# Optimization experiments

Measured on AMD Instinct MI355X. Metric: run time of the kernel, lower is better.

Reference implementation:

```python
import jax, jax.numpy as jnp
import numpy as np

TWO_THIRDS = 2.0 / 3.0
SEVENTEEN_SIXTHS = 17.0 / 6.0


def _grid():
    # torch: cat(-flip(logspace(-2,2,100)**2), [0], logspace(-2,2,100)**2) -> 201 points
    gp = jnp.logspace(-2.0, 2.0, 100, dtype=jnp.float32) ** 2
    return jnp.concatenate([-gp[::-1], jnp.zeros((1,), jnp.float32), gp])


def _trapz_w(x):
    # trapezoidal quadrature weights so that trapz(f, x) == sum(f * w)
    dx = jnp.diff(x)
    w = jnp.zeros_like(x)
    return w.at[:-1].add(0.5 * dx).at[1:].add(0.5 * dx)


def setup_inputs() -> dict:
    key = jax.random.key(0)
    k1k, kyk, kzk = jax.random.split(key, 3)
    k1 = jnp.sort(jax.random.uniform(k1k, (512,), jnp.float32, 0.01, 1.0))  # positive wavenumbers
    dy = jax.random.uniform(kyk, (64,), jnp.float32, 0.0, 50.0)  # spanwise separations [m]
    dz = jax.random.uniform(kzk, (64,), jnp.float32, 0.0, 50.0)  # vertical separations [m]
    return {
        "k1_input": k1,
        "Delta_y": dy,
        "Delta_z": dz,
        "logLengthScale": jnp.float32(np.log(0.7 * 42.0)),
        "logTimeScale": jnp.float32(np.log(3.9)),
        "logMagnitude": jnp.float32(0.0),
    }


def reference(k1_input, Delta_y, Delta_z, logLengthScale, logTimeScale, logMagnitude):
    L = jnp.exp(logLengthScale)
    T = jnpp = jnp.exp(logTimeScale)
    M = jnp.exp(logMagnitude)
    k2g = _grid()  # [201]
    k3g = _grid()  # [201]
    # broadcasted meshgrid (never materialize a 4D stacked k tensor)
    k1 = k1_input[:, None, None]   # [Nk1,1,1]
    k2 = k2g[None, :, None]        # [1,201,1]
    k3 = k3g[None, None, :]        # [1,1,201]
    kk = k1 * k1 + k2 * k2 + k3 * k3
    # EddyLifetime 'TwoThird': beta = T * (L*|k|)^{-2/3}
    beta = T * (L * jnp.sqrt(kk)) ** (-TWO_THIRDS)
    k30 = k3 + beta * k1
    kk0 = k1 * k1 + k2 * k2 + k30 * k30
    k0L = L * jnp.sqrt(kk0)
    # von Karman energy spectrum at distorted wavevector
    E0 = M * k0L ** 4 / (1.0 + k0L * k0L) ** SEVENTEEN_SIXTHS
    # RDT spectral tensor, 11-component (module uses Phi[0] for Phi11, Phi33 and Phi13)
    s = k1 * k1 + k2 * k2
    C1 = beta * k1 * k1 * (kk0 - 2.0 * k30 * k30 + beta * k1 * k30) / (kk * s)
    C2 = k2 * kk0 / s ** 1.5 * jnp.arctan2(beta * k1 * jnp.sqrt(s), kk0 - k30 * k1 * beta)
    zeta1 = C1 - (k2 / k1) * C2
    Phi11 = E0 / (4.0 * jnp.pi * kk0 * kk0) * (
        kk0 - k1 * k1 - 2.0 * k1 * k30 * zeta1 + s * zeta1 * zeta1
    )  # [Nk1,201,201]
    # double trapezoid over (k2,k3) as weighted sums
    w2 = _trapz_w(k2g)
    w3 = _trapz_w(k3g)
    F1 = jnp.einsum('aij,i,j->a', Phi11, w2, w3)  # = F3
    den = jnp.sqrt(F1 * F1)
    # exp(i(k2*dy + k3*dz)) is separable -> factor the nested loop into two einsums
    Pw = (Phi11 * w2[None, :, None] * w3[None, None, :]).astype(jnp.complex64)
    E3 = jnp.exp(1j * k3g[:, None] * Delta_z[None, :])  # [201,Nz]
    E2 = jnp.exp(1j * k2g[:, None] * Delta_y[None, :])  # [201,Ny]
    A = jnp.einsum('aij,jz->aiz', Pw, E3)   # [Nk1,201,Nz]
    I = jnp.einsum('aiz,iy->ayz', A, E2)    # [Nk1,Ny,Nz]
    return jnp.real(I) / den[:, None, None]
```

## Files before the change

kernel.cpp:

```cpp
#include <hip/hip_runtime.h>
#include <math.h>

#define BLOCK 256
#define LOG2_10 3.3219280948873623f
#define PI_F 3.14159265358979f
#define INV2PI 0.15915494309189535f
#define PW_SCALE 256.0f

#define SP 128
#define SA 128
#define FT 56

typedef _Float16 half8 __attribute__((ext_vector_type(8)));
typedef _Float16 half2v __attribute__((ext_vector_type(2)));
typedef float f32x4 __attribute__((ext_vector_type(4)));
typedef float v2f  __attribute__((ext_vector_type(2)));
typedef int   i32x4 __attribute__((ext_vector_type(4)));

__device__ __forceinline__ v2f v2(float a, float b) { v2f r; r.x = a; r.y = b; return r; }

__device__ __forceinline__ float fast_cos(float x_rev) {
    return __builtin_amdgcn_cosf(__builtin_amdgcn_fractf(x_rev));
}

__device__ __forceinline__ v2f atan2_pos_pk(float yv, v2f x) {
    float ax0 = __builtin_fabsf(x.x), ax1 = __builtin_fabsf(x.y);
    float mn0 = fminf(ax0, yv), mx0 = fmaxf(ax0, yv);
    float mn1 = fminf(ax1, yv), mx1 = fmaxf(ax1, yv);
    v2f a = v2(mn0 * __builtin_amdgcn_rcpf(mx0), mn1 * __builtin_amdgcn_rcpf(mx1));
    v2f t = a * a;
    v2f p = ((((( -0.0117212f * t + 0.05265332f) * t - 0.11643287f) * t
              + 0.19354346f) * t - 0.33262347f) * t + 0.99997726f) * a;
    float p0 = (yv > ax0) ? (1.57079632679f - p.x) : p.x;
    float p1 = (yv > ax1) ? (1.57079632679f - p.y) : p.y;
    p0 = (x.x < 0.0f) ? (3.14159265359f - p0) : p0;
    p1 = (x.y < 0.0f) ? (3.14159265359f - p1) : p1;
    return v2(p0, p1);
}

__device__ __forceinline__ float phi_pair_pk(float k1, float k1sq, float n2k1, float Ttk1,
                                             float L2, float s, float sqs, float k2sc, float g) {
    const float kk  = g * g + s;
    const float bk1 = Ttk1 * __builtin_amdgcn_exp2f((-1.0f/3.0f) * __builtin_amdgcn_logf(L2 * kk));
    const float Qh  = bk1 * g;
    const float sg  = 2.0f * s - kk;
    const float cc  = (bk1 * k1) * __builtin_amdgcn_rcpf(kk * s);
    const float yv  = bk1 * sqs;
    const float R   = bk1 * bk1 + kk;
    const v2f x   = v2(kk - Qh, kk + Qh);
    const v2f C1  = cc * v2(sg + Qh, sg - Qh);
    const v2f kk0 = v2(R - 2.0f * Qh, R + 2.0f * Qh);
    const v2f th  = atan2_pos_pk(yv, x);
    const v2f vv  = L2 * kk0 + 1.0f;
    const v2f p   = v2(__builtin_amdgcn_exp2f((-17.0f/6.0f) * __builtin_amdgcn_logf(vv.x)),
                       __builtin_amdgcn_exp2f((-17.0f/6.0f) * __builtin_amdgcn_logf(vv.y)));
    const v2f z   = C1 - k2sc * (kk0 * th);
    const v2f k30 = v2(bk1 - g, bk1 + g);
    const v2f qq  = (s * z + n2k1 * k30) * z + (kk0 - k1sq);
    const v2f r   = p * qq;
    return r.x + r.y;
}

__device__ __forceinline__ float phi_pair_cheap(float k1sq, float L2, float s, float g) {
    const float kk = g * g + s;
    const float p  = __builtin_amdgcn_exp2f((-17.0f/6.0f) *
                     __builtin_amdgcn_logf(fmaf(L2, kk, 1.0f)));
    return 2.0f * p * (kk - k1sq);
}

__global__ __launch_bounds__(BLOCK, 2)
void spectral_kernel(const float* __restrict__ k1_in,
                     const float* __restrict__ dy_in,
                     const float* __restrict__ dz_in,
                     const float* __restrict__ plogL,
                     const float* __restrict__ plogT,
                     const float* __restrict__ plogM,
                     float* __restrict__ out)
{
    __shared__ __attribute__((aligned(16))) _Float16 s_phiT[2 * 32 * SP];
    __shared__ __attribute__((aligned(16))) _Float16 s_B3T[64 * SP];
    __shared__ __attribute__((aligned(16))) _Float16 s_A2[64 * SA];
    __shared__ float  s_grid[204];
    __shared__ float2 s_gw[204];
    __shared__ float  s_dy[64], s_dz[64];
    __shared__ float  s_red[8];

    const int t    = threadIdx.x;
    const int a    = blockIdx.x;
    const int lane = t & 63;
    const int w    = t >> 6;
    const int n16  = lane & 15;
    const int quad = lane >> 4;

    const float L  = expf(plogL[0]);
    const float Tt = expf(plogT[0]);
    const float M  = expf(plogM[0]);
    const float L2 = L * L;
    const float L4 = L2 * L2;
    const float k1   = k1_in[a];
    const float k1sq = k1 * k1;
    const float n2k1 = -2.0f * k1;
    const float Ttk1 = Tt * k1;
    const float rk1  = __builtin_amdgcn_rcpf(k1);
    const float cM0  = (M * 0.25f / PI_F) * PW_SCALE * L4;

    if (t < 204) {
        int tt = min(t, 200);
        float v;
        if (tt < 100)       v = -exp2f(LOG2_10 * (-4.0f + 8.0f * (float)(99 - tt) * (1.0f/99.0f)));
        else if (tt == 100) v = 0.0f;
        else                v =  exp2f(LOG2_10 * (-4.0f + 8.0f * (float)(tt - 101) * (1.0f/99.0f)));
        s_grid[t] = v;
    }
    if (t < 64) { s_dy[t] = dy_in[t]; s_dz[t] = dz_in[t]; }
    __syncthreads();

    if (t < 204) {
        float wv = 0.0f;
        if (t == 0)          wv = 0.5f * (s_grid[1] - s_grid[0]);
        else if (t < 200)    wv = 0.5f * (s_grid[t+1] - s_grid[t-1]);
        else if (t == 200)   wv = 0.5f * (s_grid[200] - s_grid[199]);
        s_gw[t] = make_float2(s_grid[t], wv);
    }
    {
        const int jjp = lane;
        const int jj0 = 2 * jjp, jj1 = jj0 + 1;
        if (jj0 < 96) {
            const float g0 = s_grid[100 + jj0];
            const float g1 = s_grid[100 + jj1];
            const int jjg  = jjp >> 2;
            for (int m = 0; m < 16; ++m) {
                int z = w + 4 * m;
                float dzr = s_dz[z] * INV2PI;
                float c0 = (jj0 < 88) ? fast_cos(g0 * dzr) : 0.0f;
                float c1 = (jj1 < 88) ? fast_cos(g1 * dzr) : 0.0f;
                half2v pr; pr.x = (_Float16)c0; pr.y = (_Float16)c1;
                *(half2v*)&s_B3T[z * SP + ((jjg ^ (z & 7)) << 3) + (jj0 & 7)] = pr;
            }
        }
    }
    {
        float dyr = s_dy[lane] * INV2PI;
        for (int k = 0; k < 12; ++k) {
            int iip = w + 4 * k;
            int i0 = 2 * iip, i1 = i0 + 1;
            float c0 = (i0 < 88) ? fast_cos(s_grid[100 + i0] * dyr) : 0.0f;
            float c1 = (i1 < 88) ? fast_cos(s_grid[100 + i1] * dyr) : 0.0f;
            half2v pr; pr.x = (_Float16)c0; pr.y = (_Float16)c1;
            int off = lane * SA + (((iip >> 2) ^ (lane & 7)) << 3) + ((iip & 3) << 1);
            *(half2v*)&s_A2[off] = pr;
        }
    }
    __syncthreads();

    float f1 = 0.0f;
    f32x4 acc2[4];
    #pragma unroll
    for (int i = 0; i < 4; ++i) acc2[i] = (f32x4){0.f, 0.f, 0.f, 0.f};

    auto do_full = [&](int ii, int jj, int row, _Float16* bp) {
        float k2  = s_gw[100 + ii].x;
        float cM  = cM0 * (s_gw[100 + ii].y * ((ii == 0) ? 1.0f : 2.0f));
        float s   = k1sq + k2 * k2;
        float rs  = __builtin_amdgcn_rsqf(s);
        float sqs = s * rs;
        float k2sc = (k2 * rk1) * k2 * (rs * rs * rs);
        float2 gwv = s_gw[100 + jj];
        float w3s = (jj == 0) ? 0.5f * gwv.y : gwv.y;
        float val = phi_pair_pk(k1, k1sq, n2k1, Ttk1, L2, s, sqs, k2sc, gwv.x) * cM * w3s;
        f1 += val;
        bp[row * SP + (((jj >> 3) ^ (row & 7)) << 3) + (jj & 7)] = (_Float16)val;
    };
    auto do_cheap = [&](int ii, int jj, int row, _Float16* bp) {
        float k2 = s_gw[100 + ii].x;
        float cM = cM0 * (s_gw[100 + ii].y * ((ii == 0) ? 1.0f : 2.0f));
        float s  = k1sq + k2 * k2;
        float2 gwv = s_gw[100 + jj];
        float w3s = (jj == 0) ? 0.5f * gwv.y : gwv.y;
        float val = phi_pair_cheap(k1sq, L2, s, gwv.x) * cM * w3s;
        f1 += val;
        bp[row * SP + (((jj >> 3) ^ (row & 7)) << 3) + (jj & 7)] = (_Float16)val;
    };

    {
        _Float16* bp = s_phiT;
        if (t < 32) {
            half8 zz = {};
            *(half8*)&bp[t * SP + ((11 ^ (t & 7)) << 3)] = zz;
        }
        #pragma unroll 2
        for (int m = 0; m < 7; ++m) {
            int e = t + 256 * m;
            int row = e / FT, jj = e - row * FT;
            do_full(row, jj, row, bp);
        }
        #pragma unroll
        for (int m = 0; m < 4; ++m) {
            int e = t + 256 * m;
            int row = e >> 5, jj = FT + (e & 31);
            do_cheap(row, jj, row, bp);
        }
    }
    __syncthreads();

    for (int c = 0; c < 3; ++c) {
        const _Float16* rp = s_phiT + (c & 1) * (32 * SP);

        f32x4 acc1[2];
        acc1[0] = (f32x4){0.f,0.f,0.f,0.f};
        acc1[1] = (f32x4){0.f,0.f,0.f,0.f};
        {
            const int arow0 = n16;
            const int arow1 = 16 + n16;
            const int brow  = w * 16 + n16;
            #pragma unroll
            for (int ks = 0; ks < 3; ++ks) {
                int kg = ks * 4 + quad;
                half8 af0 = *(const half8*)&rp[arow0 * SP + ((kg ^ (arow0 & 7)) << 3)];
                half8 af1 = *(const half8*)&rp[arow1 * SP + ((kg ^ (arow1 & 7)) << 3)];
                half8 bf  = *(const half8*)&s_B3T[brow * SP + ((kg ^ (brow & 7)) << 3)];
                acc1[0] = __builtin_amdgcn_mfma_f32_16x16x32_f16(af0, bf, acc1[0], 0, 0, 0);
                acc1[1] = __builtin_amdgcn_mfma_f32_16x16x32_f16(af1, bf, acc1[1], 0, 0, 0);
            }
        }

        half8 bf2;
        {
            half2v hA0; hA0.x = (_Float16)acc1[0].x; hA0.y = (_Float16)acc1[0].y;
            half2v hA1; hA1.x = (_Float16)acc1[0].z; hA1.y = (_Float16)acc1[0].w;
            half2v hB0; hB0.x = (_Float16)acc1[1].x; hB0.y = (_Float16)acc1[1].y;
            half2v hB1; hB1.x = (_Float16)acc1[1].z; hB1.y = (_Float16)acc1[1].w;
            int pkA0 = __builtin_bit_cast(int, hA0);
            int pkA1 = __builtin_bit_cast(int, hA1);
            int pkB0 = __builtin_bit_cast(int, hB0);
            int pkB1 = __builtin_bit_cast(int, hB1);
            const int addr_a = (((quad & 1) << 5) + n16) << 2;
            const int addr_b = addr_a + 64;
            int a0 = __builtin_amdgcn_ds_bpermute(addr_a, pkA0);
            int b0 = __builtin_amdgcn_ds_bpermute(addr_a, pkB0);
            int a1 = __builtin_amdgcn_ds_bpermute(addr_a, pkA1);
            int b1 = __builtin_amdgcn_ds_bpermute(addr_a, pkB1);
            int a2 = __builtin_amdgcn_ds_bpermute(addr_b, pkA0);
            int b2 = __builtin_amdgcn_ds_bpermute(addr_b, pkB0);
            int a3 = __builtin_amdgcn_ds_bpermute(addr_b, pkA1);
            int b3 = __builtin_amdgcn_ds_bpermute(addr_b, pkB1);
            const bool lo = (quad < 2);
            i32x4 wv;
            wv.x = lo ? a0 : b0;
            wv.y = lo ? a1 : b1;
            wv.z = lo ? a2 : b2;
            wv.w = lo ? a3 : b3;
            bf2 = __builtin_bit_cast(half8, wv);
        }

        {
            const int G = c * 4 + quad;
            #pragma unroll
            for (int yb = 0; yb < 4; ++yb) {
                int yrow = yb * 16 + n16;
                half8 a2f = *(const half8*)&s_A2[yrow * SA + ((G ^ (yrow & 7)) << 3)];
                acc2[yb] = __builtin_amdgcn_mfma_f32_16x16x32_f16(a2f, bf2, acc2[yb], 0, 0, 0);
            }
        }

        if (c == 0) {
            _Float16* bp = s_phiT + 32 * SP;
            if (t < 32) {
                half8 zz = {};
                *(half8*)&bp[t * SP + ((11 ^ (t & 7)) << 3)] = zz;
            }
            #pragma unroll 2
            for (int m = 0; m < 6; ++m) {
                int e = t + 256 * m;
                if (e < 1344) {
                    int row = e / FT, jj = e - row * FT;
                    do_full(32 + row, jj, row, bp);
                }
            }
            #pragma unroll
            for (int m = 0; m < 6; ++m) {
                int e = t + 256 * m;
                if (e < 1472) {
                    int row, jj;
                    if (e < 768) { row = e >> 5; jj = FT + (e & 31); }
                    else { int e2 = e - 768; row = 24 + e2 / 88; jj = e2 - (row - 24) * 88; }
                    do_cheap(32 + row, jj, row, bp);
                }
            }
        } else if (c == 1) {
            _Float16* bp = s_phiT;
            if (t < 120) {
                int row, slot;
                if (t < 96) { row = 24 + t / 12; int g = t - (row - 24) * 12; slot = g ^ (row & 7); }
                else        { row = t - 96;      slot = 11 ^ (row & 7); }
                half8 zz = {};
                *(half8*)&bp[row * SP + (slot << 3)] = zz;
            }
            #pragma unroll
            for (int m = 0; m < 9; ++m) {
                int e = t + 256 * m;
                if (e < 2112) {
                    int row = e / 88, jj = e - row * 88;
                    do_cheap(64 + row, jj, row, bp);
                }
            }
        }
        __syncthreads();
    }

    float v = f1;
    #pragma unroll
    for (int off = 32; off > 0; off >>= 1) v += __shfl_down(v, off, 64);
    if (lane == 0) s_red[w] = v;
    __syncthreads();
    if (t == 0) s_red[4] = 1.0f / fabsf(s_red[0] + s_red[1] + s_red[2] + s_red[3]);
    __syncthreads();
    const float rden = s_red[4];

    float* op = out + ((size_t)a << 12) + (w * 16 + n16);
    #pragma unroll
    for (int yb = 0; yb < 4; ++yb) {
        #pragma unroll
        for (int r = 0; r < 4; ++r) {
            int y = yb * 16 + quad * 4 + r;
            op[y * 64] = acc2[yb][r] * rden;
        }
    }
}

extern "C" void kernel_launch(void* const* d_in, const int* in_sizes, int n_in,
                              void* d_out, int out_size, void* d_ws, size_t ws_size,
                              hipStream_t stream) {
    const float* k1 = (const float*)d_in[0];
    const float* dy = (const float*)d_in[1];
    const float* dz = (const float*)d_in[2];
    const float* lL = (const float*)d_in[3];
    const float* lT = (const float*)d_in[4];
    const float* lM = (const float*)d_in[5];
    float* outp = (float*)d_out;
    hipLaunchKernelGGL(spectral_kernel, dim3(512), dim3(BLOCK), 0, stream,
                       k1, dy, dz, lL, lT, lM, outp);
}
```

Before: 79.11 us.

## Process two k1 values per block with 512 threads, sharing cos tables

Each block now handles two k1 indices with 512 threads, so the cosine basis tables (B3T, A2) built in shared memory are reused across both instead of being recomputed per k1. The phi evaluation computes both k1 values per element and shares the grid and weight loads. Waves 0-3 do the MFMA work for the first k1 and waves 4-7 for the second. This halves the grid to 256 blocks and doubles the phi LDS buffer, which may lower occupancy and leave some CUs idle on a 256-CU device.

```diff
diff --git a/kernel.cpp b/kernel.cpp
--- a/kernel.cpp
+++ b/kernel.cpp
@@ -1,7 +1,7 @@
 #include <hip/hip_runtime.h>
 #include <math.h>
 
-#define BLOCK 256
+#define BLOCK 512
 #define LOG2_10 3.3219280948873623f
 #define PI_F 3.14159265358979f
 #define INV2PI 0.15915494309189535f
@@ -77,16 +77,16 @@
                      const float* __restrict__ plogM,
                      float* __restrict__ out)
 {
-    __shared__ __attribute__((aligned(16))) _Float16 s_phiT[2 * 32 * SP];
+    __shared__ __attribute__((aligned(16))) _Float16 s_phiT[2 * 2 * 32 * SP];
     __shared__ __attribute__((aligned(16))) _Float16 s_B3T[64 * SP];
     __shared__ __attribute__((aligned(16))) _Float16 s_A2[64 * SA];
     __shared__ float  s_grid[204];
     __shared__ float2 s_gw[204];
     __shared__ float  s_dy[64], s_dz[64];
-    __shared__ float  s_red[8];
+    __shared__ float  s_redA[8], s_redB[8], s_rden[2];
 
     const int t    = threadIdx.x;
-    const int a    = blockIdx.x;
+    const int a0   = blockIdx.x * 2;
     const int lane = t & 63;
     const int w    = t >> 6;
     const int n16  = lane & 15;
@@ -97,12 +97,14 @@
     const float M  = expf(plogM[0]);
     const float L2 = L * L;
     const float L4 = L2 * L2;
-    const float k1   = k1_in[a];
-    const float k1sq = k1 * k1;
-    const float n2k1 = -2.0f * k1;
-    const float Ttk1 = Tt * k1;
-    const float rk1  = __builtin_amdgcn_rcpf(k1);
-    const float cM0  = (M * 0.25f / PI_F) * PW_SCALE * L4;
+    const float k1A   = k1_in[a0];
+    const float k1B   = k1_in[a0 + 1];
+    const float k1sqA = k1A * k1A,  k1sqB = k1B * k1B;
+    const float n2k1A = -2.0f * k1A, n2k1B = -2.0f * k1B;
+    const float Ttk1A = Tt * k1A,    Ttk1B = Tt * k1B;
+    const float rk1A  = __builtin_amdgcn_rcpf(k1A);
+    const float rk1B  = __builtin_amdgcn_rcpf(k1B);
+    const float cM0   = (M * 0.25f / PI_F) * PW_SCALE * L4;
 
     if (t < 204) {
         int tt = min(t, 200);
@@ -129,8 +131,9 @@
             const float g0 = s_grid[100 + jj0];
             const float g1 = s_grid[100 + jj1];
             const int jjg  = jjp >> 2;
-            for (int m = 0; m < 16; ++m) {
-                int z = w + 4 * m;
+            #pragma unroll
+            for (int m = 0; m < 8; ++m) {
+                int z = w + 8 * m;
                 float dzr = s_dz[z] * INV2PI;
                 float c0 = (jj0 < 88) ? fast_cos(g0 * dzr) : 0.0f;
                 float c1 = (jj1 < 88) ? fast_cos(g1 * dzr) : 0.0f;
@@ -141,8 +144,9 @@
     }
     {
         float dyr = s_dy[lane] * INV2PI;
-        for (int k = 0; k < 12; ++k) {
-            int iip = w + 4 * k;
+        #pragma unroll
+        for (int k = 0; k < 6; ++k) {
+            int iip = w + 8 * k;
             int i0 = 2 * iip, i1 = i0 + 1;
             float c0 = (i0 < 88) ? fast_cos(s_grid[100 + i0] * dyr) : 0.0f;
             float c1 = (i1 < 88) ? fast_cos(s_grid[100 + i1] * dyr) : 0.0f;
@@ -153,58 +157,77 @@
     }
     __syncthreads();
 
-    float f1 = 0.0f;
+    float f1A = 0.0f, f1B = 0.0f;
     f32x4 acc2[4];
     #pragma unroll
     for (int i = 0; i < 4; ++i) acc2[i] = (f32x4){0.f, 0.f, 0.f, 0.f};
 
-    auto do_full = [&](int ii, int jj, int row, _Float16* bp) {
+    auto do_full2 = [&](int ii, int jj, int row, _Float16* bp0, _Float16* bp1) {
         float k2  = s_gw[100 + ii].x;
-        float cM  = cM0 * (s_gw[100 + ii].y * ((ii == 0) ? 1.0f : 2.0f));
-        float s   = k1sq + k2 * k2;
-        float rs  = __builtin_amdgcn_rsqf(s);
-        float sqs = s * rs;
-        float k2sc = (k2 * rk1) * k2 * (rs * rs * rs);
+        float cMw = cM0 * (s_gw[100 + ii].y * ((ii == 0) ? 1.0f : 2.0f));
         float2 gwv = s_gw[100 + jj];
-        float w3s = (jj == 0) ? 0.5f * gwv.y : gwv.y;
-        float val = phi_pair_pk(k1, k1sq, n2k1, Ttk1, L2, s, sqs, k2sc, gwv.x) * cM * w3s;
-        f1 += val;
-        bp[row * SP + (((jj >> 3) ^ (row & 7)) << 3) + (jj & 7)] = (_Float16)val;
+        float cw  = cMw * ((jj == 0) ? 0.5f * gwv.y : gwv.y);
+        float sA   = k1sqA + k2 * k2;
+        float rsA  = __builtin_amdgcn_rsqf(sA);
+        float valA = phi_pair_pk(k1A, k1sqA, n2k1A, Ttk1A, L2, sA, sA * rsA,
+                                 (k2 * rk1A) * k2 * (rsA * rsA * rsA), gwv.x) * cw;
+        float sB   = k1sqB + k2 * k2;
+        float rsB  = __builtin_amdgcn_rsqf(sB);
+        float valB = phi_pair_pk(k1B, k1sqB, n2k1B, Ttk1B, L2, sB, sB * rsB,
+                                 (k2 * rk1B) * k2 * (rsB * rsB * rsB), gwv.x) * cw;
+        f1A += valA; f1B += valB;
+        int off = row * SP + (((jj >> 3) ^ (row & 7)) << 3) + (jj & 7);
+        bp0[off] = (_Float16)valA;
+        bp1[off] = (_Float16)valB;
     };
-    auto do_cheap = [&](int ii, int jj, int row, _Float16* bp) {
-        float k2 = s_gw[100 + ii].x;
-        float cM = cM0 * (s_gw[100 + ii].y * ((ii == 0) ? 1.0f : 2.0f));
-        float s  = k1sq + k2 * k2;
+    auto do_cheap2 = [&](int ii, int jj, int row, _Float16* bp0, _Float16* bp1) {
+        float k2  = s_gw[100 + ii].x;
+        float cMw = cM0 * (s_gw[100 + ii].y * ((ii == 0) ? 1.0f : 2.0f));
         float2 gwv = s_gw[100 + jj];
-        float w3s = (jj == 0) ? 0.5f * gwv.y : gwv.y;
-        float val = phi_pair_cheap(k1sq, L2, s, gwv.x) * cM * w3s;
-        f1 += val;
-        bp[row * SP + (((jj >> 3) ^ (row & 7)) << 3) + (jj & 7)] = (_Float16)val;
+        float cw  = cMw * ((jj == 0) ? 0.5f * gwv.y : gwv.y);
+        float valA = phi_pair_cheap(k1sqA, L2, k1sqA + k2 * k2, gwv.x) * cw;
+        float valB = phi_pair_cheap(k1sqB, L2, k1sqB + k2 * k2, gwv.x) * cw;
+        f1A += valA; f1B += valB;
+        int off = row * SP + (((jj >> 3) ^ (row & 7)) << 3) + (jj & 7);
+        bp0[off] = (_Float16)valA;
+        bp1[off] = (_Float16)valB;
     };
 
+    _Float16* pA0 = s_phiT;
+    _Float16* pA1 = s_phiT + 32 * SP;
+    _Float16* pB0 = s_phiT + 64 * SP;
+    _Float16* pB1 = s_phiT + 96 * SP;
+
     {
-        _Float16* bp = s_phiT;
         if (t < 32) {
             half8 zz = {};
-            *(half8*)&bp[t * SP + ((11 ^ (t & 7)) << 3)] = zz;
-        }
-        #pragma unroll 2
-        for (int m = 0; m < 7; ++m) {
-            int e = t + 256 * m;
-            int row = e / FT, jj = e - row * FT;
-            do_full(row, jj, row, bp);
+            int off = t * SP + ((11 ^ (t & 7)) << 3);
+            *(half8*)&pA0[off] = zz;
+            *(half8*)&pB0[off] = zz;
         }
         #pragma unroll
         for (int m = 0; m < 4; ++m) {
-            int e = t + 256 * m;
+            int e = t + 512 * m;
+            if (e < 1792) {
+                int row = e / FT, jj = e - row * FT;
+                do_full2(row, jj, row, pA0, pB0);
+            }
+        }
+        #pragma unroll
+        for (int m = 0; m < 2; ++m) {
+            int e = t + 512 * m;
             int row = e >> 5, jj = FT + (e & 31);
-            do_cheap(row, jj, row, bp);
-        }
-    }
-    __syncthreads();
+            do_cheap2(row, jj, row, pA0, pB0);
+        }
+    }
+    __syncthreads();
+
+    const int ia = w >> 2;
+    const int zb = w & 3;
+    const float* k1sel = ia ? &k1B : &k1A;
 
     for (int c = 0; c < 3; ++c) {
-        const _Float16* rp = s_phiT + (c & 1) * (32 * SP);
+        const _Float16* rp = s_phiT + ia * (64 * SP) + (c & 1) * (32 * SP);
 
         f32x4 acc1[2];
         acc1[0] = (f32x4){0.f,0.f,0.f,0.f};
@@ -212,7 +235,7 @@
         {
             const int arow0 = n16;
             const int arow1 = 16 + n16;
-            const int brow  = w * 16 + n16;
+            const int brow  = zb * 16 + n16;
             #pragma unroll
             for (int ks = 0; ks < 3; ++ks) {
                 int kg = ks * 4 + quad;
@@ -236,20 +259,20 @@
             int pkB1 = __builtin_bit_cast(int, hB1);
             const int addr_a = (((quad & 1) << 5) + n16) << 2;
             const int addr_b = addr_a + 64;
-            int a0 = __builtin_amdgcn_ds_bpermute(addr_a, pkA0);
-            int b0 = __builtin_amdgcn_ds_bpermute(addr_a, pkB0);
-            int a1 = __builtin_amdgcn_ds_bpermute(addr_a, pkA1);
-            int b1 = __builtin_amdgcn_ds_bpermute(addr_a, pkB1);
-            int a2 = __builtin_amdgcn_ds_bpermute(addr_b, pkA0);
-            int b2 = __builtin_amdgcn_ds_bpermute(addr_b, pkB0);
-            int a3 = __builtin_amdgcn_ds_bpermute(addr_b, pkA1);
-            int b3 = __builtin_amdgcn_ds_bpermute(addr_b, pkB1);
+            int a0v = __builtin_amdgcn_ds_bpermute(addr_a, pkA0);
+            int b0v = __builtin_amdgcn_ds_bpermute(addr_a, pkB0);
+            int a1v = __builtin_amdgcn_ds_bpermute(addr_a, pkA1);
+            int b1v = __builtin_amdgcn_ds_bpermute(addr_a, pkB1);
+            int a2v = __builtin_amdgcn_ds_bpermute(addr_b, pkA0);
+            int b2v = __builtin_amdgcn_ds_bpermute(addr_b, pkB0);
+            int a3v = __builtin_amdgcn_ds_bpermute(addr_b, pkA1);
+            int b3v = __builtin_amdgcn_ds_bpermute(addr_b, pkB1);
             const bool lo = (quad < 2);
             i32x4 wv;
-            wv.x = lo ? a0 : b0;
-            wv.y = lo ? a1 : b1;
-            wv.z = lo ? a2 : b2;
-            wv.w = lo ? a3 : b3;
+            wv.x = lo ? a0v : b0v;
+            wv.y = lo ? a1v : b1v;
+            wv.z = lo ? a2v : b2v;
+            wv.w = lo ? a3v : b3v;
             bf2 = __builtin_bit_cast(half8, wv);
         }
 
@@ -264,60 +287,70 @@
         }
 
         if (c == 0) {
-            _Float16* bp = s_phiT + 32 * SP;
             if (t < 32) {
                 half8 zz = {};
-                *(half8*)&bp[t * SP + ((11 ^ (t & 7)) << 3)] = zz;
-            }
-            #pragma unroll 2
-            for (int m = 0; m < 6; ++m) {
-                int e = t + 256 * m;
+                int off = t * SP + ((11 ^ (t & 7)) << 3);
+                *(half8*)&pA1[off] = zz;
+                *(half8*)&pB1[off] = zz;
+            }
+            #pragma unroll
+            for (int m = 0; m < 3; ++m) {
+                int e = t + 512 * m;
                 if (e < 1344) {
                     int row = e / FT, jj = e - row * FT;
-                    do_full(32 + row, jj, row, bp);
+                    do_full2(32 + row, jj, row, pA1, pB1);
                 }
             }
             #pragma unroll
-            for (int m = 0; m < 6; ++m) {
-                int e = t + 256 * m;
+            for (int m = 0; m < 3; ++m) {
+                int e = t + 512 * m;
                 if (e < 1472) {
                     int row, jj;
                     if (e < 768) { row = e >> 5; jj = FT + (e & 31); }
                     else { int e2 = e - 768; row = 24 + e2 / 88; jj = e2 - (row - 24) * 88; }
-                    do_cheap(32 + row, jj, row, bp);
+                    do_cheap2(32 + row, jj, row, pA1, pB1);
                 }
             }
         } else if (c == 1) {
-            _Float16* bp = s_phiT;
             if (t < 120) {
                 int row, slot;
                 if (t < 96) { row = 24 + t / 12; int g = t - (row - 24) * 12; slot = g ^ (row & 7); }
                 else        { row = t - 96;      slot = 11 ^ (row & 7); }
                 half8 zz = {};
-                *(half8*)&bp[row * SP + (slot << 3)] = zz;
-            }
-            #pragma unroll
-            for (int m = 0; m < 9; ++m) {
-                int e = t + 256 * m;
+                *(half8*)&pA0[row * SP + (slot << 3)] = zz;
+                *(half8*)&pB0[row * SP + (slot << 3)] = zz;
+            }
+            #pragma unroll
+            for (int m = 0; m < 5; ++m) {
+                int e = t + 512 * m;
                 if (e < 2112) {
                     int row = e / 88, jj = e - row * 88;
-                    do_cheap(64 + row, jj, row, bp);
+                    do_cheap2(64 + row, jj, row, pA0, pB0);
                 }
             }
         }
         __syncthreads();
     }
 
-    float v = f1;
+    float vA = f1A, vB = f1B;
     #pragma unroll
-    for (int off = 32; off > 0; off >>= 1) v += __shfl_down(v, off, 64);
-    if (lane == 0) s_red[w] = v;
-    __syncthreads();
-    if (t == 0) s_red[4] = 1.0f / fabsf(s_red[0] + s_red[1] + s_red[2] + s_red[3]);
-    __syncthreads();
-    const float rden = s_red[4];
-
-    float* op = out + ((size_t)a << 12) + (w * 16 + n16);
+    for (int off = 32; off > 0; off >>= 1) {
+        vA += __shfl_down(vA, off, 64);
+        vB += __shfl_down(vB, off, 64);
+    }
+    if (lane == 0) { s_redA[w] = vA; s_redB[w] = vB; }
+    __syncthreads();
+    if (t == 0) {
+        float sA = 0.0f, sB = 0.0f;
+        #pragma unroll
+        for (int i = 0; i < 8; ++i) { sA += s_redA[i]; sB += s_redB[i]; }
+        s_rden[0] = 1.0f / fabsf(sA);
+        s_rden[1] = 1.0f / fabsf(sB);
+    }
+    __syncthreads();
+    const float rden = s_rden[ia];
+
+    float* op = out + ((size_t)(a0 + ia) << 12) + (zb * 16 + n16);
     #pragma unroll
     for (int yb = 0; yb < 4; ++yb) {
         #pragma unroll
@@ -326,6 +359,7 @@
             op[y * 64] = acc2[yb][r] * rden;
         }
     }
+    (void)k1sel;
 }
 
 extern "C" void kernel_launch(void* const* d_in, const int* in_sizes, int n_in,
@@ -338,6 +372,6 @@
     const float* lT = (const float*)d_in[4];
     const float* lM = (const float*)d_in[5];
     float* outp = (float*)d_out;
-    hipLaunchKernelGGL(spectral_kernel, dim3(512), dim3(BLOCK), 0, stream,
+    hipLaunchKernelGGL(spectral_kernel, dim3(256), dim3(BLOCK), 0, stream,
                        k1, dy, dz, lL, lT, lM, outp);
 }
```

After: 75.69 us. -4.3%, faster.
